# Kernel tuning notes

Measured on AMD Instinct MI355X. Metric: run time of the kernel, lower is better.

Reference implementation:

```python
import jax, jax.numpy as jnp
import numpy as np

E = 500000          # num edges
N = 50000           # num nodes
D_IN = 32           # n_input_features (edge feature dim)
D_HID = 128         # n_hidden_features
D_NODE = 16         # n_node_features; MLP head outputs D_NODE**2


def _linear_params(key, d_in, d_out):
    kw, kb = jax.random.split(key)
    bound = 1.0 / np.sqrt(d_in)
    W = jax.random.uniform(kw, (d_out, d_in), jnp.float32, -bound, bound)
    b = jax.random.uniform(kb, (d_out,), jnp.float32, -bound, bound)
    return W, b


def setup_inputs() -> dict:
    key = jax.random.key(0)
    k1, k2, k3, k4, k5, k6, k7 = jax.random.split(key, 7)
    edge_features = jax.random.normal(k1, (E, D_IN), jnp.float32)
    node_features = jax.random.normal(k2, (N, D_NODE), jnp.float32)
    edge_index = jax.random.randint(k3, (E, 2), 0, N, jnp.int64 if jax.config.jax_enable_x64 else jnp.int32)
    W1, b1 = _linear_params(k4, D_IN, D_HID)
    W2, b2 = _linear_params(k5, D_HID, D_HID)
    W3, b3 = _linear_params(k6, D_HID, D_HID)
    W4, b4 = _linear_params(k7, D_HID, D_NODE * D_NODE)
    return {
        "edge_features": edge_features,
        "node_features": node_features,
        "W1": W1, "b1": b1, "W2": W2, "b2": b2,
        "W3": W3, "b3": b3, "W4": W4, "b4": b4,
        "edge_index": edge_index,
    }


def reference(edge_features, node_features, W1, b1, W2, b2, W3, b3, W4, b4, edge_index):
    neighbors = edge_index[:, 1]                       # [E]
    ef = edge_features[neighbors]                      # [E, D_IN] gather
    nf = node_features[neighbors]                      # [E, D_NODE] gather
    h = jax.nn.relu(ef @ W1.T + b1)                    # [E, D_HID]
    h = jax.nn.relu(h @ W2.T + b2)
    h = jax.nn.relu(h @ W3.T + b3)
    edge_out = h @ W4.T + b4                           # [E, D_NODE**2]
    d = nf.shape[-1]
    message = edge_out.reshape(-1, d, d)               # [E, d, d]
    # per-edge matrix-vector product: (message @ nf[..., None]).squeeze(-1)
    return jnp.einsum("eij,ej->ei", message, nf)       # [E, d]
```

## Files before the change

kernel.cpp:

```cpp
#include <hip/hip_runtime.h>
#include <stdint.h>

typedef __attribute__((ext_vector_type(8))) short short8;
typedef __attribute__((ext_vector_type(4))) float f32x4;
typedef __attribute__((ext_vector_type(16))) float f32x16;
typedef __attribute__((ext_vector_type(4))) unsigned int u32x4;

#define NE 500000
#define NN 50000
#define NT32 1563
#define SC_BLOCKS 2048
#define SC_THREADS (SC_BLOCKS * 256)

__device__ __forceinline__ unsigned int f2bf1(float f) {
  unsigned int u = __builtin_bit_cast(unsigned int, f);
  u += 0x7FFFu + ((u >> 16) & 1u);
  return u >> 16;
}
__device__ __forceinline__ unsigned int packbf2(float lo, float hi) {
  return f2bf1(lo) | (f2bf1(hi) << 16);
}
__device__ __forceinline__ short8 pack8(f32x4 a, f32x4 b) {
  short8 r;
  r[0] = (short)f2bf1(a[0]); r[1] = (short)f2bf1(a[1]);
  r[2] = (short)f2bf1(a[2]); r[3] = (short)f2bf1(a[3]);
  r[4] = (short)f2bf1(b[0]); r[5] = (short)f2bf1(b[1]);
  r[6] = (short)f2bf1(b[2]); r[7] = (short)f2bf1(b[3]);
  return r;
}

__global__ __launch_bounds__(512, 2) void mlp_kernel(
    const float* __restrict__ ef, const float* __restrict__ nfeat,
    const float* __restrict__ W1, const float* __restrict__ b1,
    const float* __restrict__ W2, const float* __restrict__ b2,
    const float* __restrict__ W3, const float* __restrict__ b3,
    const float* __restrict__ W4, const float* __restrict__ b4,
    float* __restrict__ Rout) {
  __shared__ __align__(16) unsigned short wlds[69632];
  __shared__ __align__(16) float blds[640];

  const int t = threadIdx.x;
  const int lane = t & 63, w = t >> 6;
  const int cn = lane & 31;
  const int h  = lane >> 5;

  const int g = w * 256 + blockIdx.x;
  const bool active = (g < NT32);
  const int node = (active ? g * 32 : 0) + cn;
  const int nodeL = node < NN ? node : NN - 1;

  const float* xp = ef + (size_t)nodeL * 32;
  f32x4 x00 = *(const f32x4*)(xp + h * 8);
  f32x4 x01 = *(const f32x4*)(xp + h * 8 + 4);
  f32x4 x10 = *(const f32x4*)(xp + 16 + h * 8);
  f32x4 x11 = *(const f32x4*)(xp + 16 + h * 8 + 4);
  f32x4 nfa = *(const f32x4*)(nfeat + (size_t)nodeL * 16 + 4 * h);
  f32x4 nfb = *(const f32x4*)(nfeat + (size_t)nodeL * 16 + 8 + 4 * h);

  #pragma unroll
  for (int i = 0; i < 17; ++i) {
    int idx = t + i * 512;
    int f = idx >> 6, l = idx & 63;
    int r = l & 31, hh = l >> 5;
    const float *pa, *pb;
    if (f < 8) {
      int ob = f >> 1, s = f & 1;
      const float* base = W1 + (ob * 32 + r) * 32 + s * 16 + hh * 8;
      pa = base; pb = base + 4;
    } else {
      const float* W; int i2;
      if (f < 40)      { W = W2; i2 = f - 8;  }
      else if (f < 72) { W = W3; i2 = f - 40; }
      else             { W = W4; i2 = f - 72; }
      int ob = i2 >> 3, s = i2 & 7;
      const float* base = W + (ob * 32 + r) * 128
                        + (s >> 1) * 32 + (s & 1) * 16 + 4 * hh;
      pa = base; pb = base + 8;
    }
    *(short8*)&wlds[f * 512 + l * 8] = pack8(*(const f32x4*)pa, *(const f32x4*)pb);
  }
  if (t < 160) {
    const float* s = t < 32 ? b1 + t * 4
                   : t < 64 ? b2 + (t - 32) * 4
                   : t < 96 ? b3 + (t - 64) * 4
                   :          b4 + (t - 96) * 4;
    ((f32x4*)blds)[t] = *(const f32x4*)s;
  }
  __syncthreads();

  if (!active) return;

  auto initacc = [&](int boff) -> f32x16 {
    f32x16 a;
    #pragma unroll
    for (int q = 0; q < 4; ++q) {
      f32x4 cv = *(const f32x4*)&blds[boff + 4 * h + 8 * q];
      a[4*q+0] = cv[0]; a[4*q+1] = cv[1]; a[4*q+2] = cv[2]; a[4*q+3] = cv[3];
    }
    return a;
  };
  auto frag = [&](int f) -> short8 {
    return *(const short8*)&wlds[f * 512 + lane * 8];
  };

  short8 bx0 = pack8(x00, x01);
  short8 bx1 = pack8(x10, x11);
  f32x16 acc[4];
  #pragma unroll
  for (int ob = 0; ob < 4; ++ob) {
    f32x16 c = initacc(ob * 32);
    c = __builtin_amdgcn_mfma_f32_32x32x16_bf16(frag(ob * 2 + 0), bx0, c, 0, 0, 0);
    c = __builtin_amdgcn_mfma_f32_32x32x16_bf16(frag(ob * 2 + 1), bx1, c, 0, 0, 0);
    acc[ob] = c;
  }

  short8 bf[8];
  auto transition = [&]() {
    #pragma unroll
    for (int s = 0; s < 8; ++s) {
      const f32x16 A = acc[s >> 1];
      const int b0 = 8 * (s & 1);
      u32x4 u = { packbf2(fmaxf(A[b0+0],0.f), fmaxf(A[b0+1],0.f)),
                  packbf2(fmaxf(A[b0+2],0.f), fmaxf(A[b0+3],0.f)),
                  packbf2(fmaxf(A[b0+4],0.f), fmaxf(A[b0+5],0.f)),
                  packbf2(fmaxf(A[b0+6],0.f), fmaxf(A[b0+7],0.f)) };
      bf[s] = __builtin_bit_cast(short8, u);
    }
  };
  transition();

  #pragma unroll
  for (int L = 0; L < 2; ++L) {
    const int wbase = 8 + L * 32, bbase = 128 + L * 128;
    f32x16 nacc[4];
    #pragma unroll
    for (int ob = 0; ob < 4; ++ob) {
      f32x16 c = initacc(bbase + ob * 32);
      #pragma unroll
      for (int s = 0; s < 8; ++s)
        c = __builtin_amdgcn_mfma_f32_32x32x16_bf16(frag(wbase + ob * 8 + s), bf[s], c, 0, 0, 0);
      nacc[ob] = c;
    }
    acc[0] = nacc[0]; acc[1] = nacc[1]; acc[2] = nacc[2]; acc[3] = nacc[3];
    transition();
  }

  float o0=0.f,o1=0.f,o2=0.f,o3=0.f,o4=0.f,o5=0.f,o6=0.f,o7=0.f;
  #pragma unroll
  for (int nb4 = 0; nb4 < 8; ++nb4) {
    f32x16 d = initacc(384 + nb4 * 32);
    #pragma unroll
    for (int s = 0; s < 8; ++s)
      d = __builtin_amdgcn_mfma_f32_32x32x16_bf16(frag(72 + nb4 * 8 + s), bf[s], d, 0, 0, 0);
    float p0 = d[0]*nfa[0] + d[1]*nfa[1] + d[2]*nfa[2] + d[3]*nfa[3]
             + d[4]*nfb[0] + d[5]*nfb[1] + d[6]*nfb[2] + d[7]*nfb[3];
    float p1 = d[8]*nfa[0] + d[9]*nfa[1] + d[10]*nfa[2] + d[11]*nfa[3]
             + d[12]*nfb[0]+ d[13]*nfb[1]+ d[14]*nfb[2]+ d[15]*nfb[3];
    p0 += __shfl_xor(p0, 32, 64);
    p1 += __shfl_xor(p1, 32, 64);
    int rs = nb4 - h * 4;
    o0 = (rs == 0) ? p0 : o0;  o1 = (rs == 0) ? p1 : o1;
    o2 = (rs == 1) ? p0 : o2;  o3 = (rs == 1) ? p1 : o3;
    o4 = (rs == 2) ? p0 : o4;  o5 = (rs == 2) ? p1 : o5;
    o6 = (rs == 3) ? p0 : o6;  o7 = (rs == 3) ? p1 : o7;
  }
  if (node < NN) {
    f32x4 oa = { o0, o1, o2, o3 };
    f32x4 ob_ = { o4, o5, o6, o7 };
    *(f32x4*)(Rout + (size_t)node * 16 + h * 8)     = oa;
    *(f32x4*)(Rout + (size_t)node * 16 + h * 8 + 4) = ob_;
  }
}

__global__ __launch_bounds__(256) void scatter_kernel(
    const int* __restrict__ eidx, const float* __restrict__ Rbuf,
    float* __restrict__ out) {
  const int tid = blockIdx.x * 256 + threadIdx.x;
  const int total = NE * 4;
  const int i0 = tid;
  const int i1 = tid + SC_THREADS;
  const int i2 = tid + 2 * SC_THREADS;
  const int i3 = tid + 3 * SC_THREADS;
  const bool d3 = (i3 < total);

  int nA = eidx[((i0 >> 2) << 1) + 1];
  int nB = eidx[((i1 >> 2) << 1) + 1];
  int nC = eidx[((i2 >> 2) << 1) + 1];
  int nD = d3 ? eidx[((i3 >> 2) << 1) + 1] : 0;

  f32x4 vA = *(const f32x4*)(Rbuf + nA * 16 + (i0 & 3) * 4);
  f32x4 vB = *(const f32x4*)(Rbuf + nB * 16 + (i1 & 3) * 4);
  f32x4 vC = *(const f32x4*)(Rbuf + nC * 16 + (i2 & 3) * 4);
  f32x4 vD = d3 ? *(const f32x4*)(Rbuf + nD * 16 + (i3 & 3) * 4) : f32x4{0,0,0,0};

  *(f32x4*)(out + (size_t)i0 * 4) = vA;
  *(f32x4*)(out + (size_t)i1 * 4) = vB;
  *(f32x4*)(out + (size_t)i2 * 4) = vC;
  if (d3) *(f32x4*)(out + (size_t)i3 * 4) = vD;
}

extern "C" void kernel_launch(void* const* d_in, const int* in_sizes, int n_in,
                              void* d_out, int out_size, void* d_ws, size_t ws_size,
                              hipStream_t stream) {
  const float* ef = (const float*)d_in[0];
  const float* nf = (const float*)d_in[1];
  const float* W1 = (const float*)d_in[2];
  const float* b1 = (const float*)d_in[3];
  const float* W2 = (const float*)d_in[4];
  const float* b2 = (const float*)d_in[5];
  const float* W3 = (const float*)d_in[6];
  const float* b3 = (const float*)d_in[7];
  const float* W4 = (const float*)d_in[8];
  const float* b4 = (const float*)d_in[9];
  const int* eidx = (const int*)d_in[10];

  float* Rbuf = (float*)d_ws;
  float* out = (float*)d_out;

  hipLaunchKernelGGL(mlp_kernel, dim3(256), dim3(512), 0, stream,
                     ef, nf, W1, b1, W2, b2, W3, b3, W4, b4, Rbuf);
  hipLaunchKernelGGL(scatter_kernel, dim3(SC_BLOCKS), dim3(256), 0, stream,
                     eidx, Rbuf, out);
}
```

Before: 36.40 us.

## Pre-pack bf16 weight fragments in a separate kernel and read them from global/L2

Adds a prep kernel that converts the MLP weights to bf16 MFMA fragment layout once per call into workspace. The MLP kernel stops staging about 136KB of weights in LDS per block and instead loads fragments from global memory (L2-resident). It uses 256-thread blocks with more blocks and more occupancy, and partially unrolls the final layer loop to cut register pressure. The aim is to remove the per-block weight conversion and LDS staging overhead, at the cost of an extra launch and repeated global/L2 fragment reads inside the MFMA loops.

```diff
diff --git a/kernel.cpp b/kernel.cpp
--- a/kernel.cpp
+++ b/kernel.cpp
@@ -9,6 +9,7 @@
 #define NE 500000
 #define NN 50000
 #define NT32 1563
+#define MLP_BLOCKS 391
 #define SC_BLOCKS 2048
 #define SC_THREADS (SC_BLOCKS * 256)
 
@@ -29,14 +30,37 @@
   return r;
 }
 
-__global__ __launch_bounds__(512, 2) void mlp_kernel(
+__global__ __launch_bounds__(256) void prep_weights(
+    const float* __restrict__ W1, const float* __restrict__ W2,
+    const float* __restrict__ W3, const float* __restrict__ W4,
+    unsigned short* __restrict__ wf) {
+  int idx = blockIdx.x * 256 + threadIdx.x;
+  if (idx >= 8704) return;
+  int f = idx >> 6, l = idx & 63;
+  int r = l & 31, hh = l >> 5;
+  const float *pa, *pb;
+  if (f < 8) {
+    int ob = f >> 1, s = f & 1;
+    const float* base = W1 + (ob * 32 + r) * 32 + s * 16 + hh * 8;
+    pa = base; pb = base + 4;
+  } else {
+    const float* W; int i2;
+    if (f < 40)      { W = W2; i2 = f - 8;  }
+    else if (f < 72) { W = W3; i2 = f - 40; }
+    else             { W = W4; i2 = f - 72; }
+    int ob = i2 >> 3, s = i2 & 7;
+    const float* base = W + (ob * 32 + r) * 128
+                      + (s >> 1) * 32 + (s & 1) * 16 + 4 * hh;
+    pa = base; pb = base + 8;
+  }
+  *(short8*)&wf[f * 512 + l * 8] = pack8(*(const f32x4*)pa, *(const f32x4*)pb);
+}
+
+__global__ __launch_bounds__(256, 3) void mlp_kernel(
     const float* __restrict__ ef, const float* __restrict__ nfeat,
-    const float* __restrict__ W1, const float* __restrict__ b1,
-    const float* __restrict__ W2, const float* __restrict__ b2,
-    const float* __restrict__ W3, const float* __restrict__ b3,
-    const float* __restrict__ W4, const float* __restrict__ b4,
-    float* __restrict__ Rout) {
-  __shared__ __align__(16) unsigned short wlds[69632];
+    const float* __restrict__ b1, const float* __restrict__ b2,
+    const float* __restrict__ b3, const float* __restrict__ b4,
+    const unsigned short* __restrict__ wf, float* __restrict__ Rout) {
   __shared__ __align__(16) float blds[640];
 
   const int t = threadIdx.x;
@@ -44,7 +68,7 @@
   const int cn = lane & 31;
   const int h  = lane >> 5;
 
-  const int g = w * 256 + blockIdx.x;
+  const int g = blockIdx.x * 4 + w;
   const bool active = (g < NT32);
   const int node = (active ? g * 32 : 0) + cn;
   const int nodeL = node < NN ? node : NN - 1;
@@ -57,28 +81,6 @@
   f32x4 nfa = *(const f32x4*)(nfeat + (size_t)nodeL * 16 + 4 * h);
   f32x4 nfb = *(const f32x4*)(nfeat + (size_t)nodeL * 16 + 8 + 4 * h);
 
-  #pragma unroll
-  for (int i = 0; i < 17; ++i) {
-    int idx = t + i * 512;
-    int f = idx >> 6, l = idx & 63;
-    int r = l & 31, hh = l >> 5;
-    const float *pa, *pb;
-    if (f < 8) {
-      int ob = f >> 1, s = f & 1;
-      const float* base = W1 + (ob * 32 + r) * 32 + s * 16 + hh * 8;
-      pa = base; pb = base + 4;
-    } else {
-      const float* W; int i2;
-      if (f < 40)      { W = W2; i2 = f - 8;  }
-      else if (f < 72) { W = W3; i2 = f - 40; }
-      else             { W = W4; i2 = f - 72; }
-      int ob = i2 >> 3, s = i2 & 7;
-      const float* base = W + (ob * 32 + r) * 128
-                        + (s >> 1) * 32 + (s & 1) * 16 + 4 * hh;
-      pa = base; pb = base + 8;
-    }
-    *(short8*)&wlds[f * 512 + l * 8] = pack8(*(const f32x4*)pa, *(const f32x4*)pb);
-  }
   if (t < 160) {
     const float* s = t < 32 ? b1 + t * 4
                    : t < 64 ? b2 + (t - 32) * 4
@@ -100,7 +102,7 @@
     return a;
   };
   auto frag = [&](int f) -> short8 {
-    return *(const short8*)&wlds[f * 512 + lane * 8];
+    return *(const short8*)&wf[f * 512 + lane * 8];
   };
 
   short8 bx0 = pack8(x00, x01);
@@ -146,7 +148,7 @@
   }
 
   float o0=0.f,o1=0.f,o2=0.f,o3=0.f,o4=0.f,o5=0.f,o6=0.f,o7=0.f;
-  #pragma unroll
+  #pragma unroll 2
   for (int nb4 = 0; nb4 < 8; ++nb4) {
     f32x16 d = initacc(384 + nb4 * 32);
     #pragma unroll
@@ -214,11 +216,14 @@
   const float* b4 = (const float*)d_in[9];
   const int* eidx = (const int*)d_in[10];
 
-  float* Rbuf = (float*)d_ws;
+  unsigned short* wfrag = (unsigned short*)d_ws;
+  float* Rbuf = (float*)((char*)d_ws + 139264);
   float* out = (float*)d_out;
 
-  hipLaunchKernelGGL(mlp_kernel, dim3(256), dim3(512), 0, stream,
-                     ef, nf, W1, b1, W2, b2, W3, b3, W4, b4, Rbuf);
+  hipLaunchKernelGGL(prep_weights, dim3(34), dim3(256), 0, stream,
+                     W1, W2, W3, W4, wfrag);
+  hipLaunchKernelGGL(mlp_kernel, dim3(MLP_BLOCKS), dim3(256), 0, stream,
+                     ef, nf, b1, b2, b3, b4, wfrag, Rbuf);
   hipLaunchKernelGGL(scatter_kernel, dim3(SC_BLOCKS), dim3(256), 0, stream,
                      eidx, Rbuf, out);
 }
```

New measurement: 52.82 us. 1.45x slower.
